# Optimization experiments

Measured on AMD Instinct MI355X. Metric: run time of the kernel, lower is better.

Reference implementation:

```python
import jax, jax.numpy as jnp
import numpy as np

VOCAB = 2048


def setup_inputs() -> dict:
    key = jax.random.key(0)
    kx, kc = jax.random.split(key)
    x = jax.random.randint(kx, (8, 2048), 0, VOCAB, dtype=jnp.int64)
    C = jax.random.normal(kc, (4, 4), dtype=jnp.float32) * 0.02
    return {"x": x, "C": C}


def reference(x, C):
    B, T = x.shape
    k = C.shape[0]
    # one-hot embedding, zero-padded with k-1 leading positions (pad rows are all-zero vectors)
    emb = jax.nn.one_hot(x, VOCAB, dtype=jnp.float32)            # [B, T, V]
    padded = jnp.concatenate(
        [jnp.zeros((B, k - 1, VOCAB), dtype=jnp.float32), emb], axis=1
    )                                                             # [B, T+k-1, V]
    # windows[b, t, i, :] = padded[b, t + k - 1 - i, :]  (unfold + permute + flip)
    windows = jnp.stack(
        [padded[:, k - 1 - i : k - 1 - i + T, :] for i in range(k)], axis=2
    )                                                             # [B, T, k, V]
    q_window = windows[:, -1, :, :]                               # [B, k, V]
    # equality-match matrix over the vocab dimension
    match = jnp.einsum('biv,btjv->btij', q_window, windows)       # [B, T, k, k]
    scores = jnp.einsum('btij,ij->bt', match, C)                  # [B, T]
    # mask out the last (query) position
    scores = scores.at[:, -1].set(jnp.float32(-1e9))
    attn = jax.nn.softmax(scores, axis=-1)                        # [B, T]
    values = windows[:, :, 0, :]                                  # [B, T, V] (== emb)
    out = jnp.einsum('bt,btv->bv', attn, values)                  # [B, V]
    return out
```

## Files before the change

### kernel.cpp

```cpp
#include <hip/hip_runtime.h>

#define T 2048
#define BLK 256
#define K 4

__global__ __launch_bounds__(BLK) void constrained_attn_kernel(
    const int* __restrict__ x, const float* __restrict__ C, float* __restrict__ out)
{
    __shared__ int   xs[T];
    __shared__ float outs[T];
    __shared__ float red[BLK / 64];

    const int b   = blockIdx.x;
    const int tid = threadIdx.x;
    const int* xb = x + b * T;

    for (int t = tid; t < T; t += BLK) {
        xs[t]   = xb[t];
        outs[t] = 0.0f;
    }
    __syncthreads();

    const int q0 = xs[T - 1], q1 = xs[T - 2], q2 = xs[T - 3], q3 = xs[T - 4];
    float c[16];
#pragma unroll
    for (int k = 0; k < 16; ++k) c[k] = C[k];

    float sc[T / BLK];
    float lmax = -1e30f;
#pragma unroll
    for (int r = 0; r < T / BLK; ++r) {
        const int t = tid + r * BLK;
        float s = 0.0f;
#pragma unroll
        for (int j = 0; j < K; ++j) {
            const int tj = t - j;
            if (tj >= 0) {
                const int xv = xs[tj];
                s += (xv == q0 ? c[0 * 4 + j] : 0.0f);
                s += (xv == q1 ? c[1 * 4 + j] : 0.0f);
                s += (xv == q2 ? c[2 * 4 + j] : 0.0f);
                s += (xv == q3 ? c[3 * 4 + j] : 0.0f);
            }
        }
        if (t == T - 1) s = -1e9f;
        sc[r] = s;
        lmax = fmaxf(lmax, s);
    }

#pragma unroll
    for (int off = 32; off > 0; off >>= 1)
        lmax = fmaxf(lmax, __shfl_xor(lmax, off));
    if ((tid & 63) == 0) red[tid >> 6] = lmax;
    __syncthreads();
    float m = red[0];
#pragma unroll
    for (int w = 1; w < BLK / 64; ++w) m = fmaxf(m, red[w]);

    float lsum = 0.0f;
#pragma unroll
    for (int r = 0; r < T / BLK; ++r) {
        sc[r] = __expf(sc[r] - m);
        lsum += sc[r];
    }
#pragma unroll
    for (int off = 32; off > 0; off >>= 1)
        lsum += __shfl_xor(lsum, off);
    __syncthreads();
    if ((tid & 63) == 0) red[tid >> 6] = lsum;
    __syncthreads();
    float tot = 0.0f;
#pragma unroll
    for (int w = 0; w < BLK / 64; ++w) tot += red[w];
    const float inv = 1.0f / tot;

#pragma unroll
    for (int r = 0; r < T / BLK; ++r) {
        const int t = tid + r * BLK;
        atomicAdd(&outs[xs[t]], sc[r] * inv);
    }
    __syncthreads();

    float* ob = out + b * T;
    for (int v = tid; v < T; v += BLK)
        ob[v] = outs[v];
}

extern "C" void kernel_launch(void* const* d_in, const int* in_sizes, int n_in,
                              void* d_out, int out_size, void* d_ws, size_t ws_size,
                              hipStream_t stream) {
    const int*   x = (const int*)d_in[0];
    const float* C = (const float*)d_in[1];
    float*     out = (float*)d_out;
    const int B = in_sizes[0] / T;
    constrained_attn_kernel<<<B, BLK, 0, stream>>>(x, C, out);
}
```

Before: 11.66 us.

## Assign contiguous positions per thread and load tokens directly into registers

Each thread now owns 8 contiguous positions and reads its tokens plus a 3-element halo with vectorized int4 global loads. This removes the shared-memory token staging and its barrier. The softmax sum uses a separate region of the reduction buffer, which drops one __syncthreads, and the output write-back becomes float4. The trade-off is redundant halo loads and a layout where the scatter atomics come from contiguous rather than strided positions.

```diff
diff --git a/kernel.cpp b/kernel.cpp
--- a/kernel.cpp
+++ b/kernel.cpp
@@ -1,50 +1,56 @@
 #include <hip/hip_runtime.h>
 
-#define T 2048
+#define T   2048
 #define BLK 256
-#define K 4
+#define PT  (T / BLK)
 
 __global__ __launch_bounds__(BLK) void constrained_attn_kernel(
     const int* __restrict__ x, const float* __restrict__ C, float* __restrict__ out)
 {
-    __shared__ int   xs[T];
     __shared__ float outs[T];
-    __shared__ float red[BLK / 64];
+    __shared__ float red[8];
 
-    const int b   = blockIdx.x;
-    const int tid = threadIdx.x;
-    const int* xb = x + b * T;
+    const int b    = blockIdx.x;
+    const int tid  = threadIdx.x;
+    const int* xb  = x + b * T;
+    const int base = tid * PT;
 
-    for (int t = tid; t < T; t += BLK) {
-        xs[t]   = xb[t];
-        outs[t] = 0.0f;
-    }
-    __syncthreads();
+    const int4 q4 = *(const int4*)(xb + T - 4);
+    const int4 v0 = *(const int4*)(xb + base);
+    const int4 v1 = *(const int4*)(xb + base + 4);
+    int4 vp = make_int4(-1, -1, -1, -1);
+    if (tid > 0) vp = *(const int4*)(xb + base - 4);
+    const float4 c0 = *(const float4*)(C + 0);
+    const float4 c1 = *(const float4*)(C + 4);
+    const float4 c2 = *(const float4*)(C + 8);
+    const float4 c3 = *(const float4*)(C + 12);
 
-    const int q0 = xs[T - 1], q1 = xs[T - 2], q2 = xs[T - 3], q3 = xs[T - 4];
-    float c[16];
-#pragma unroll
-    for (int k = 0; k < 16; ++k) c[k] = C[k];
+    for (int v = tid; v < T; v += BLK) outs[v] = 0.0f;
 
-    float sc[T / BLK];
+    const int q0 = q4.w, q1 = q4.z, q2 = q4.y, q3 = q4.x;
+    const float c[16] = {c0.x, c0.y, c0.z, c0.w,
+                         c1.x, c1.y, c1.z, c1.w,
+                         c2.x, c2.y, c2.z, c2.w,
+                         c3.x, c3.y, c3.z, c3.w};
+    const int arr[PT + 3] = {vp.y, vp.z, vp.w,
+                             v0.x, v0.y, v0.z, v0.w,
+                             v1.x, v1.y, v1.z, v1.w};
+
+    float sc[PT];
     float lmax = -1e30f;
 #pragma unroll
-    for (int r = 0; r < T / BLK; ++r) {
-        const int t = tid + r * BLK;
+    for (int k = 0; k < PT; ++k) {
         float s = 0.0f;
 #pragma unroll
-        for (int j = 0; j < K; ++j) {
-            const int tj = t - j;
-            if (tj >= 0) {
-                const int xv = xs[tj];
-                s += (xv == q0 ? c[0 * 4 + j] : 0.0f);
-                s += (xv == q1 ? c[1 * 4 + j] : 0.0f);
-                s += (xv == q2 ? c[2 * 4 + j] : 0.0f);
-                s += (xv == q3 ? c[3 * 4 + j] : 0.0f);
-            }
+        for (int j = 0; j < 4; ++j) {
+            const int xv = arr[3 + k - j];
+            s += (xv == q0 ? c[0  + j] : 0.0f);
+            s += (xv == q1 ? c[4  + j] : 0.0f);
+            s += (xv == q2 ? c[8  + j] : 0.0f);
+            s += (xv == q3 ? c[12 + j] : 0.0f);
         }
-        if (t == T - 1) s = -1e9f;
-        sc[r] = s;
+        if (base + k == T - 1) s = -1e9f;
+        sc[k] = s;
         lmax = fmaxf(lmax, s);
     }
 
@@ -53,37 +59,29 @@
         lmax = fmaxf(lmax, __shfl_xor(lmax, off));
     if ((tid & 63) == 0) red[tid >> 6] = lmax;
     __syncthreads();
-    float m = red[0];
-#pragma unroll
-    for (int w = 1; w < BLK / 64; ++w) m = fmaxf(m, red[w]);
+    const float m = fmaxf(fmaxf(red[0], red[1]), fmaxf(red[2], red[3]));
 
     float lsum = 0.0f;
 #pragma unroll
-    for (int r = 0; r < T / BLK; ++r) {
-        sc[r] = __expf(sc[r] - m);
-        lsum += sc[r];
+    for (int k = 0; k < PT; ++k) {
+        sc[k] = __expf(sc[k] - m);
+        lsum += sc[k];
     }
 #pragma unroll
     for (int off = 32; off > 0; off >>= 1)
         lsum += __shfl_xor(lsum, off);
+    if ((tid & 63) == 0) red[4 + (tid >> 6)] = lsum;
     __syncthreads();
-    if ((tid & 63) == 0) red[tid >> 6] = lsum;
-    __syncthreads();
-    float tot = 0.0f;
-#pragma unroll
-    for (int w = 0; w < BLK / 64; ++w) tot += red[w];
-    const float inv = 1.0f / tot;
+    const float inv = 1.0f / (red[4] + red[5] + red[6] + red[7]);
 
 #pragma unroll
-    for (int r = 0; r < T / BLK; ++r) {
-        const int t = tid + r * BLK;
-        atomicAdd(&outs[xs[t]], sc[r] * inv);
-    }
+    for (int k = 0; k < PT; ++k)
+        atomicAdd(&outs[arr[3 + k]], sc[k] * inv);
     __syncthreads();
 
     float* ob = out + b * T;
-    for (int v = tid; v < T; v += BLK)
-        ob[v] = outs[v];
+    *(float4*)(ob + base)     = *(const float4*)(outs + base);
+    *(float4*)(ob + base + 4) = *(const float4*)(outs + base + 4);
 }
 
 extern "C" void kernel_launch(void* const* d_in, const int* in_sizes, int n_in,
```

Measured after the change: 10.65 us. 1.1x faster.
